# Kernel optimization log

Measured on AMD Instinct MI355X. Metric: run time of the kernel, lower is better.

## Reference

```python
import jax, jax.numpy as jnp
import numpy as np

H = 1024  # hidden_size
NH = 16   # num_attention_heads
HD = H // NH  # head_dim = 64


def setup_inputs() -> dict:
    key = jax.random.key(0)
    ks = jax.random.split(key, 9)
    s = 0.02
    return {
        "hidden_states": jax.random.normal(ks[0], (2, 2048, H), dtype=jnp.float32),
        "Wq": jax.random.normal(ks[1], (H, H), dtype=jnp.float32) * s,
        "bq": jnp.zeros((H,), dtype=jnp.float32),
        "Wk": jax.random.normal(ks[2], (H, H), dtype=jnp.float32) * s,
        "bk": jnp.zeros((H,), dtype=jnp.float32),
        "Wv": jax.random.normal(ks[3], (H, H), dtype=jnp.float32) * s,
        "bv": jnp.zeros((H,), dtype=jnp.float32),
        "Wo": jax.random.normal(ks[4], (H, H), dtype=jnp.float32) * s,
        "bo": jnp.zeros((H,), dtype=jnp.float32),
    }


def reference(hidden_states, Wq, bq, Wk, bk, Wv, bv, Wo, bo):
    B, S, _ = hidden_states.shape
    scale = 1.0 / np.sqrt(HD)
    # torch Linear: x @ W.T + b
    q = (hidden_states @ Wq.T + bq).reshape(B, S, NH, HD).transpose(0, 2, 1, 3)
    k = (hidden_states @ Wk.T + bk).reshape(B, S, NH, HD).transpose(0, 2, 1, 3)
    v = (hidden_states @ Wv.T + bv).reshape(B, S, NH, HD).transpose(0, 2, 1, 3)
    # full (non-causal) attention; tiled_matmul == plain matmul mathematically
    scores = jnp.einsum("bhqd,bhkd->bhqk", q, k) * scale
    attn = jax.nn.softmax(scores, axis=-1)
    out = jnp.einsum("bhqk,bhkd->bhqd", attn, v)
    out = out.transpose(0, 2, 1, 3).reshape(B, S, H)
    return out @ Wo.T + bo
```

## Files before the change

### kernel.cpp

```cpp
#include <hip/hip_runtime.h>

typedef unsigned short u16;
typedef __attribute__((ext_vector_type(8))) short bf16x8;
typedef __attribute__((ext_vector_type(4))) float f32x4;
typedef __attribute__((ext_vector_type(4))) unsigned int u32x4;

#define SEQ 2048
#define HID 1024
#define NHEAD 16
#define HDIM 64
#define MTOK 4096

#define MFMA16(a,b,c) __builtin_amdgcn_mfma_f32_16x16x32_bf16(a,b,c,0,0,0)

__device__ __forceinline__ u16 f2bf(float f){
  unsigned int u = __builtin_bit_cast(unsigned int, f);
  u += 0x7fffu + ((u >> 16) & 1u);
  return (u16)(u >> 16);
}

__device__ __forceinline__ void gload16(const u16* g, u16* l){
  __builtin_amdgcn_global_load_lds((const __attribute__((address_space(1))) void*)g,
                                   (__attribute__((address_space(3))) void*)l, 16, 0, 0);
}

__global__ __launch_bounds__(256) void cast_all(
    const float* __restrict__ hs, const float* __restrict__ Wq,
    const float* __restrict__ Wk, const float* __restrict__ Wv,
    const float* __restrict__ Wo, u16* __restrict__ Xb,
    u16* __restrict__ Wqkv, u16* __restrict__ Wob){
  int y = blockIdx.y;
  int i = blockIdx.x * 256 + threadIdx.x;
  const float* src; u16* dst; size_t i8;
  if (y < 4){ src = hs; dst = Xb; i8 = (size_t)y * 131072 + i; }
  else {
    int w = y - 4;
    src = (w == 0) ? Wq : (w == 1) ? Wk : (w == 2) ? Wv : Wo;
    dst = (w == 3) ? Wob : (Wqkv + (size_t)w * HID * HID);
    i8 = i;
  }
  const float4* p = (const float4*)src;
  float4 a = p[2*i8], b = p[2*i8+1];
  u32x4 o;
  o.x = (unsigned)f2bf(a.x) | ((unsigned)f2bf(a.y) << 16);
  o.y = (unsigned)f2bf(a.z) | ((unsigned)f2bf(a.w) << 16);
  o.z = (unsigned)f2bf(b.x) | ((unsigned)f2bf(b.y) << 16);
  o.w = (unsigned)f2bf(b.z) | ((unsigned)f2bf(b.w) << 16);
  ((u32x4*)dst)[i8] = o;
}

__global__ __launch_bounds__(256) void gemm_qkv(
    const u16* __restrict__ Xb, const u16* __restrict__ Wqkv,
    const float* __restrict__ bq, const float* __restrict__ bk, const float* __restrict__ bv,
    u16* __restrict__ Qb, u16* __restrict__ Kb, u16* __restrict__ Vtb)
{
  __shared__ __attribute__((aligned(16))) u16 pool[24576];
  u16* const AsP = pool;
  u16* const BsP = pool + 12288;
  const int tid = threadIdx.x, wave = tid >> 6, lane = tid & 63;
  const int m0 = blockIdx.x * 128, n0 = blockIdx.y * 128;
  const int wr = (wave >> 1) * 64, wc = (wave & 1) * 64;
  const int lr = lane & 15, lg = lane >> 4, kseg = lg * 8;

#define STAGE_Q(k0, buf) do { \
  _Pragma("unroll") \
  for (int i_ = 0; i_ < 2; i_++){ \
    int u_ = (i_*4 + wave) * 64 + lane; \
    int row_ = u_ >> 2, cu_ = u_ & 3; \
    gload16(Xb   + (size_t)(m0 + row_) * HID + (k0) + cu_*8, AsP + (buf)*4096 + (i_*4 + wave) * 512); \
    gload16(Wqkv + (size_t)(n0 + row_) * HID + (k0) + cu_*8, BsP + (buf)*4096 + (i_*4 + wave) * 512); \
  } } while(0)

  f32x4 zero = {0.f, 0.f, 0.f, 0.f};
  f32x4 acc[4][4];
#pragma unroll
  for (int i = 0; i < 4; i++)
#pragma unroll
    for (int j = 0; j < 4; j++) acc[i][j] = zero;

  STAGE_Q(0, 0);
  STAGE_Q(32, 1);
  for (int t = 0; t < 32; t++){
    if (t < 31) { asm volatile("s_waitcnt vmcnt(4)" ::: "memory"); }
    else        { asm volatile("s_waitcnt vmcnt(0)" ::: "memory"); }
    __builtin_amdgcn_s_barrier();
    __builtin_amdgcn_sched_barrier(0);
    if (t < 30) STAGE_Q((t+2)*32, (t+2)%3);
    int cur = t % 3;
    const u16* Ac = AsP + cur*4096; const u16* Bc = BsP + cur*4096;
    bf16x8 af[4], bfr[4];
#pragma unroll
    for (int m = 0; m < 4; m++) af[m]  = *(const bf16x8*)&Ac[(wr + m*16 + lr)*32 + kseg];
#pragma unroll
    for (int n = 0; n < 4; n++) bfr[n] = *(const bf16x8*)&Bc[(wc + n*16 + lr)*32 + kseg];
    __builtin_amdgcn_s_setprio(1);
#pragma unroll
    for (int m = 0; m < 4; m++)
#pragma unroll
      for (int n = 0; n < 4; n++)
        acc[m][n] = MFMA16(af[m], bfr[n], acc[m][n]);
    __builtin_amdgcn_s_setprio(0);
  }

  __syncthreads();
  const int sel = n0 >> 10;
  const float* bias = (sel == 0) ? bq : (sel == 1) ? bk : bv;
  const float qscale = (sel == 0) ? 0.18033688011f : 1.0f;
  u16* const Ct = pool;
#pragma unroll
  for (int n = 0; n < 4; n++){
    int colL = wc + n*16 + lr;
    float bb = bias[(n0 + colL) & 1023];
#pragma unroll
    for (int m = 0; m < 4; m++){
      int rowL = wr + m*16 + lg*4;
#pragma unroll
      for (int r = 0; r < 4; r++){
        u16 v = f2bf((acc[m][n][r] + bb) * qscale);
        if (sel == 2) Ct[(size_t)colL*136 + rowL + r] = v;
        else          Ct[(size_t)(rowL + r)*136 + colL] = v;
      }
    }
  }
  __syncthreads();
  const int hbase = (n0 & 1023) >> 6;
  if (sel < 2){
    int sl = tid & 127, hh = tid >> 7;
    int rowg = m0 + sl, b = rowg >> 11, s = rowg & 2047;
    u16* dst = ((sel == 0) ? Qb : Kb) + (((size_t)(b*16 + hbase + hh))*SEQ + s)*HDIM;
    const u16* srcl = Ct + (size_t)sl*136 + hh*64;
#pragma unroll
    for (int j = 0; j < 8; j++)
      *(u32x4*)(dst + j*8) = *(const u32x4*)(srcl + j*8);
  } else {
    int dcol = tid >> 1, sh = tid & 1;
    int b = m0 >> 11, s0 = (m0 & 2047) + sh*64;
    int h = hbase + (dcol >> 6), d = dcol & 63;
    u16* dst = Vtb + (((size_t)(b*16 + h))*HDIM + d)*SEQ + s0;
    const u16* srcl = Ct + (size_t)dcol*136 + sh*64;
#pragma unroll
    for (int j = 0; j < 8; j++)
      *(u32x4*)(dst + j*8) = *(const u32x4*)(srcl + j*8);
  }
}

__global__ __launch_bounds__(256) void attn_kernel(
    const u16* __restrict__ Qb, const u16* __restrict__ Kb, const u16* __restrict__ Vtb,
    u16* __restrict__ AOb)
{
  __shared__ __attribute__((aligned(16))) u16 Ks[3][64*64];
  __shared__ __attribute__((aligned(16))) u16 Vs[3][64*64];
  const int tid = threadIdx.x, wave = tid >> 6, lane = tid & 63;
  const int lr = lane & 15, lg = lane >> 4;
  const int bid = blockIdx.x;
  const int xcd = bid & 7, slot = bid >> 3;
  const int bh = xcd*4 + (slot >> 4);
  const int q0 = (slot & 15) * 128;
  const u16* Qh = Qb  + (size_t)bh * SEQ * HDIM;
  const u16* Kh = Kb  + (size_t)bh * SEQ * HDIM;
  const u16* Vh = Vtb + (size_t)bh * HDIM * SEQ;

#define STAGE_KV(kv0, buf) do { \
  _Pragma("unroll") \
  for (int i_ = 0; i_ < 2; i_++){ \
    int u_ = i_*256 + tid; \
    int r_ = u_ >> 3, s_ = u_ & 7, ss_ = s_ ^ (r_ & 7); \
    gload16(Kh + (size_t)((kv0) + r_) * HDIM + ss_*8, &Ks[buf][u_*8]); \
    gload16(Vh + (size_t)r_ * SEQ + (kv0) + ss_*8,    &Vs[buf][u_*8]); \
  } } while(0)

  bf16x8 qf[2][2];
#pragma unroll
  for (int qb = 0; qb < 2; qb++)
#pragma unroll
    for (int ks = 0; ks < 2; ks++)
      qf[qb][ks] = *(const bf16x8*)&Qh[(size_t)(q0 + wave*32 + qb*16 + lr) * HDIM + ks*32 + lg*8];

  f32x4 zero = {0.f, 0.f, 0.f, 0.f};
  f32x4 acc[2][4];
#pragma unroll
  for (int qb = 0; qb < 2; qb++)
#pragma unroll
    for (int fd = 0; fd < 4; fd++) acc[qb][fd] = zero;
  float m_c[2] = {-1e30f, -1e30f};
  float l_c[2] = {0.f, 0.f};

  STAGE_KV(0, 0);
  STAGE_KV(64, 1);
  for (int t = 0; t < 32; t++){
    if (t < 31) { asm volatile("s_waitcnt vmcnt(4)" ::: "memory"); }
    else        { asm volatile("s_waitcnt vmcnt(0)" ::: "memory"); }
    __builtin_amdgcn_s_barrier();
    __builtin_amdgcn_sched_barrier(0);
    if (t < 30) STAGE_KV((t+2)*64, (t+2)%3);
    int cur = t % 3;
    const u16* Kc = &Ks[cur][0];
    const u16* Vc = &Vs[cur][0];

    f32x4 st[2][4];
    __builtin_amdgcn_s_setprio(1);
#pragma unroll
    for (int f = 0; f < 4; f++){
      bf16x8 kf0 = *(const bf16x8*)&Kc[(f*16 + lr)*64 + ((lg     ^ (lr & 7)) * 8)];
      bf16x8 kf1 = *(const bf16x8*)&Kc[(f*16 + lr)*64 + (((4+lg) ^ (lr & 7)) * 8)];
      st[0][f] = MFMA16(kf0, qf[0][0], zero);
      st[0][f] = MFMA16(kf1, qf[0][1], st[0][f]);
      st[1][f] = MFMA16(kf0, qf[1][0], zero);
      st[1][f] = MFMA16(kf1, qf[1][1], st[1][f]);
    }
    __builtin_amdgcn_s_setprio(0);

    float pm[2];
#pragma unroll
    for (int qb = 0; qb < 2; qb++){
      float a0 = fmaxf(fmaxf(st[qb][0][0], st[qb][0][1]), fmaxf(st[qb][0][2], st[qb][0][3]));
      float a1 = fmaxf(fmaxf(st[qb][1][0], st[qb][1][1]), fmaxf(st[qb][1][2], st[qb][1][3]));
      float a2 = fmaxf(fmaxf(st[qb][2][0], st[qb][2][1]), fmaxf(st[qb][2][2], st[qb][2][3]));
      float a3 = fmaxf(fmaxf(st[qb][3][0], st[qb][3][1]), fmaxf(st[qb][3][2], st[qb][3][3]));
      pm[qb] = fmaxf(fmaxf(a0, a1), fmaxf(a2, a3));
    }
    int need = (pm[0] > m_c[0] + 11.5f) || (pm[1] > m_c[1] + 11.5f);
    if (__any(need)){
#pragma unroll
      for (int qb = 0; qb < 2; qb++){
        float mt = pm[qb];
        mt = fmaxf(mt, __shfl_xor(mt, 16));
        mt = fmaxf(mt, __shfl_xor(mt, 32));
        float mn = fmaxf(m_c[qb], mt);
        float al = __builtin_amdgcn_exp2f(m_c[qb] - mn);
        m_c[qb] = mn;
        l_c[qb] *= al;
        float r0 = __shfl(al, lg*4 + 0), r1 = __shfl(al, lg*4 + 1);
        float r2 = __shfl(al, lg*4 + 2), r3 = __shfl(al, lg*4 + 3);
#pragma unroll
        for (int fd = 0; fd < 4; fd++){
          acc[qb][fd][0] *= r0; acc[qb][fd][1] *= r1;
          acc[qb][fd][2] *= r2; acc[qb][fd][3] *= r3;
        }
      }
    }

    bf16x8 pa[2][2];
#pragma unroll
    for (int qb = 0; qb < 2; qb++){
      unsigned w[4][2];
      float ssum = 0.f;
#pragma unroll
      for (int f = 0; f < 4; f++){
        float p0 = __builtin_amdgcn_exp2f(st[qb][f][0] - m_c[qb]);
        float p1 = __builtin_amdgcn_exp2f(st[qb][f][1] - m_c[qb]);
        float p2 = __builtin_amdgcn_exp2f(st[qb][f][2] - m_c[qb]);
        float p3 = __builtin_amdgcn_exp2f(st[qb][f][3] - m_c[qb]);
        ssum += (p0 + p1) + (p2 + p3);
        asm("v_cvt_pk_bf16_f32 %0, %1, %2" : "=v"(w[f][0]) : "v"(p0), "v"(p1));
        asm("v_cvt_pk_bf16_f32 %0, %1, %2" : "=v"(w[f][1]) : "v"(p2), "v"(p3));
      }
      l_c[qb] += ssum;
#pragma unroll
      for (int ks = 0; ks < 2; ks++){
        u32x4 aw;
#pragma unroll
        for (int rr = 0; rr < 2; rr++){
          unsigned X = w[2*ks][rr], Y = w[2*ks+1][rr];
          asm("v_permlane32_swap_b32 %0, %1" : "+v"(X), "+v"(Y));
          asm("v_permlane16_swap_b32 %0, %1" : "+v"(X), "+v"(Y));
          aw[rr] = X; aw[2 + rr] = Y;
        }
        pa[qb][ks] = __builtin_bit_cast(bf16x8, aw);
      }
    }

    __builtin_amdgcn_s_setprio(1);
#pragma unroll
    for (int ks = 0; ks < 2; ks++)
#pragma unroll
      for (int fd = 0; fd < 4; fd++){
        bf16x8 vf = *(const bf16x8*)&Vc[(fd*16 + lr)*64 + (((ks*4 + lg) ^ (lr & 7)) * 8)];
        acc[0][fd] = MFMA16(pa[0][ks], vf, acc[0][fd]);
        acc[1][fd] = MFMA16(pa[1][ks], vf, acc[1][fd]);
      }
    __builtin_amdgcn_s_setprio(0);
  }

  const int b = bh >> 4, h = bh & 15;
#pragma unroll
  for (int qb = 0; qb < 2; qb++){
    float lt = l_c[qb];
    lt += __shfl_xor(lt, 16);
    lt += __shfl_xor(lt, 32);
    float li[4];
#pragma unroll
    for (int r = 0; r < 4; r++) li[r] = 1.0f / __shfl(lt, lg*4 + r);
#pragma unroll
    for (int fd = 0; fd < 4; fd++){
      int d = h*64 + fd*16 + lr;
#pragma unroll
      for (int r = 0; r < 4; r++){
        int s = q0 + wave*32 + qb*16 + lg*4 + r;
        AOb[((size_t)(b*SEQ + s))*HID + d] = f2bf(acc[qb][fd][r] * li[r]);
      }
    }
  }
}

__global__ __launch_bounds__(256) void gemm_out(
    const u16* __restrict__ Ab, const u16* __restrict__ Wob,
    const float* __restrict__ bo, float* __restrict__ Out)
{
  __shared__ __attribute__((aligned(16))) u16 As[3][64*32];
  __shared__ __attribute__((aligned(16))) u16 Bs[3][128*32];
  const int tid = threadIdx.x, wave = tid >> 6, lane = tid & 63;
  const int m0 = blockIdx.x * 64, n0 = blockIdx.y * 128;
  const int wr = (wave >> 1) * 32, wc = (wave & 1) * 64;
  const int lr = lane & 15, lg = lane >> 4, kseg = lg * 8;

#define STAGE_O(k0, buf) do { \
  { int u_ = wave*64 + lane; \
    int row_ = u_ >> 2, cu_ = u_ & 3; \
    gload16(Ab + (size_t)(m0 + row_) * HID + (k0) + cu_*8, &As[buf][wave * 512]); } \
  _Pragma("unroll") \
  for (int i_ = 0; i_ < 2; i_++){ \
    int u_ = (i_*4 + wave) * 64 + lane; \
    int row_ = u_ >> 2, cu_ = u_ & 3; \
    gload16(Wob + (size_t)(n0 + row_) * HID + (k0) + cu_*8, &Bs[buf][(i_*4 + wave) * 512]); \
  } } while(0)

  f32x4 zero = {0.f, 0.f, 0.f, 0.f};
  f32x4 acc[2][4];
#pragma unroll
  for (int i = 0; i < 2; i++)
#pragma unroll
    for (int j = 0; j < 4; j++) acc[i][j] = zero;

  STAGE_O(0, 0);
  STAGE_O(32, 1);
  for (int t = 0; t < 32; t++){
    if (t < 31) { asm volatile("s_waitcnt vmcnt(3)" ::: "memory"); }
    else        { asm volatile("s_waitcnt vmcnt(0)" ::: "memory"); }
    __builtin_amdgcn_s_barrier();
    __builtin_amdgcn_sched_barrier(0);
    if (t < 30) STAGE_O((t+2)*32, (t+2)%3);
    int cur = t % 3;
    const u16* Ac = As[cur]; const u16* Bc = Bs[cur];
    bf16x8 af[2], bfr[4];
#pragma unroll
    for (int m = 0; m < 2; m++) af[m]  = *(const bf16x8*)&Ac[(wr + m*16 + lr)*32 + kseg];
#pragma unroll
    for (int n = 0; n < 4; n++) bfr[n] = *(const bf16x8*)&Bc[(wc + n*16 + lr)*32 + kseg];
    __builtin_amdgcn_s_setprio(1);
#pragma unroll
    for (int m = 0; m < 2; m++)
#pragma unroll
      for (int n = 0; n < 4; n++)
        acc[m][n] = MFMA16(af[m], bfr[n], acc[m][n]);
    __builtin_amdgcn_s_setprio(0);
  }

#pragma unroll
  for (int n = 0; n < 4; n++){
    int col = n0 + wc + n*16 + lr;
    float bb = bo[col];
#pragma unroll
    for (int m = 0; m < 2; m++){
      int rbase = m0 + wr + m*16 + lg*4;
#pragma unroll
      for (int r = 0; r < 4; r++)
        Out[(size_t)(rbase + r) * HID + col] = acc[m][n][r] + bb;
    }
  }
}

extern "C" void kernel_launch(void* const* d_in, const int* in_sizes, int n_in,
                              void* d_out, int out_size, void* d_ws, size_t ws_size,
                              hipStream_t stream){
  const float* hs = (const float*)d_in[0];
  const float* Wq = (const float*)d_in[1];
  const float* bq = (const float*)d_in[2];
  const float* Wk = (const float*)d_in[3];
  const float* bk = (const float*)d_in[4];
  const float* Wv = (const float*)d_in[5];
  const float* bv = (const float*)d_in[6];
  const float* Wo = (const float*)d_in[7];
  const float* bo = (const float*)d_in[8];
  float* Out = (float*)d_out;

  u16* Xb   = (u16*)d_ws;
  u16* Wqkv = Xb   + (size_t)MTOK * HID;
  u16* Wob  = Wqkv + (size_t)3 * HID * HID;
  u16* Qb   = Wob  + (size_t)HID * HID;
  u16* Kb   = Qb   + (size_t)MTOK * HID;
  u16* Vtb  = Kb   + (size_t)MTOK * HID;
  u16* AOb  = Vtb  + (size_t)MTOK * HID;

  cast_all<<<dim3(512, 8), 256, 0, stream>>>(hs, Wq, Wk, Wv, Wo, Xb, Wqkv, Wob);
  gemm_qkv<<<dim3(MTOK/128, 3*HID/128), 256, 0, stream>>>(Xb, Wqkv, bq, bk, bv, Qb, Kb, Vtb);
  attn_kernel<<<512, 256, 0, stream>>>(Qb, Kb, Vtb, AOb);
  gemm_out<<<dim3(MTOK/64, HID/128), 256, 0, stream>>>(AOb, Wob, bo, Out);
}
```

Baseline: 204.7 us.

## Load K/V tiles directly from global into registers, drop LDS staging

```diff
diff --git a/kernel.cpp b/kernel.cpp
--- a/kernel.cpp
+++ b/kernel.cpp
@@ -148,33 +148,40 @@
     const u16* __restrict__ Qb, const u16* __restrict__ Kb, const u16* __restrict__ Vtb,
     u16* __restrict__ AOb)
 {
-  __shared__ __attribute__((aligned(16))) u16 Ks[3][64*64];
-  __shared__ __attribute__((aligned(16))) u16 Vs[3][64*64];
   const int tid = threadIdx.x, wave = tid >> 6, lane = tid & 63;
   const int lr = lane & 15, lg = lane >> 4;
   const int bid = blockIdx.x;
   const int xcd = bid & 7, slot = bid >> 3;
   const int bh = xcd*4 + (slot >> 4);
-  const int q0 = (slot & 15) * 128;
+  const int q0 = (slot & 15) * 128 + wave*32;
   const u16* Qh = Qb  + (size_t)bh * SEQ * HDIM;
   const u16* Kh = Kb  + (size_t)bh * SEQ * HDIM;
   const u16* Vh = Vtb + (size_t)bh * HDIM * SEQ;
-
-#define STAGE_KV(kv0, buf) do { \
+  const u16* kb = Kh + lr*HDIM + lg*8;
+  const u16* vb = Vh + (size_t)lr*SEQ + lg*8;
+
+#define LOADK(D, kv0_) do { \
   _Pragma("unroll") \
-  for (int i_ = 0; i_ < 2; i_++){ \
-    int u_ = i_*256 + tid; \
-    int r_ = u_ >> 3, s_ = u_ & 7, ss_ = s_ ^ (r_ & 7); \
-    gload16(Kh + (size_t)((kv0) + r_) * HDIM + ss_*8, &Ks[buf][u_*8]); \
-    gload16(Vh + (size_t)r_ * SEQ + (kv0) + ss_*8,    &Vs[buf][u_*8]); \
-  } } while(0)
+  for (int f_ = 0; f_ < 4; f_++) \
+    _Pragma("unroll") \
+    for (int h_ = 0; h_ < 2; h_++) \
+      D[f_*2 + h_] = *(const u32x4*)(kb + (size_t)(kv0_)*HDIM + f_*16*HDIM + h_*32); \
+  } while(0)
+
+#define LOADV(kv0_) do { \
+  _Pragma("unroll") \
+  for (int fd_ = 0; fd_ < 4; fd_++) \
+    _Pragma("unroll") \
+    for (int ks_ = 0; ks_ < 2; ks_++) \
+      vv[fd_*2 + ks_] = *(const u32x4*)(vb + (size_t)fd_*16*SEQ + (kv0_) + ks_*32); \
+  } while(0)
 
   bf16x8 qf[2][2];
 #pragma unroll
   for (int qb = 0; qb < 2; qb++)
 #pragma unroll
     for (int ks = 0; ks < 2; ks++)
-      qf[qb][ks] = *(const bf16x8*)&Qh[(size_t)(q0 + wave*32 + qb*16 + lr) * HDIM + ks*32 + lg*8];
+      qf[qb][ks] = *(const bf16x8*)&Qh[(size_t)(q0 + qb*16 + lr) * HDIM + ks*32 + lg*8];
 
   f32x4 zero = {0.f, 0.f, 0.f, 0.f};
   f32x4 acc[2][4];
@@ -185,101 +192,97 @@
   float m_c[2] = {-1e30f, -1e30f};
   float l_c[2] = {0.f, 0.f};
 
-  STAGE_KV(0, 0);
-  STAGE_KV(64, 1);
-  for (int t = 0; t < 32; t++){
-    if (t < 31) { asm volatile("s_waitcnt vmcnt(4)" ::: "memory"); }
-    else        { asm volatile("s_waitcnt vmcnt(0)" ::: "memory"); }
-    __builtin_amdgcn_s_barrier();
-    __builtin_amdgcn_sched_barrier(0);
-    if (t < 30) STAGE_KV((t+2)*64, (t+2)%3);
-    int cur = t % 3;
-    const u16* Kc = &Ks[cur][0];
-    const u16* Vc = &Vs[cur][0];
-
-    f32x4 st[2][4];
-    __builtin_amdgcn_s_setprio(1);
-#pragma unroll
-    for (int f = 0; f < 4; f++){
-      bf16x8 kf0 = *(const bf16x8*)&Kc[(f*16 + lr)*64 + ((lg     ^ (lr & 7)) * 8)];
-      bf16x8 kf1 = *(const bf16x8*)&Kc[(f*16 + lr)*64 + (((4+lg) ^ (lr & 7)) * 8)];
-      st[0][f] = MFMA16(kf0, qf[0][0], zero);
-      st[0][f] = MFMA16(kf1, qf[0][1], st[0][f]);
-      st[1][f] = MFMA16(kf0, qf[1][0], zero);
-      st[1][f] = MFMA16(kf1, qf[1][1], st[1][f]);
-    }
-    __builtin_amdgcn_s_setprio(0);
-
-    float pm[2];
-#pragma unroll
-    for (int qb = 0; qb < 2; qb++){
-      float a0 = fmaxf(fmaxf(st[qb][0][0], st[qb][0][1]), fmaxf(st[qb][0][2], st[qb][0][3]));
-      float a1 = fmaxf(fmaxf(st[qb][1][0], st[qb][1][1]), fmaxf(st[qb][1][2], st[qb][1][3]));
-      float a2 = fmaxf(fmaxf(st[qb][2][0], st[qb][2][1]), fmaxf(st[qb][2][2], st[qb][2][3]));
-      float a3 = fmaxf(fmaxf(st[qb][3][0], st[qb][3][1]), fmaxf(st[qb][3][2], st[qb][3][3]));
-      pm[qb] = fmaxf(fmaxf(a0, a1), fmaxf(a2, a3));
-    }
-    int need = (pm[0] > m_c[0] + 11.5f) || (pm[1] > m_c[1] + 11.5f);
-    if (__any(need)){
-#pragma unroll
-      for (int qb = 0; qb < 2; qb++){
-        float mt = pm[qb];
-        mt = fmaxf(mt, __shfl_xor(mt, 16));
-        mt = fmaxf(mt, __shfl_xor(mt, 32));
-        float mn = fmaxf(m_c[qb], mt);
-        float al = __builtin_amdgcn_exp2f(m_c[qb] - mn);
-        m_c[qb] = mn;
-        l_c[qb] *= al;
-        float r0 = __shfl(al, lg*4 + 0), r1 = __shfl(al, lg*4 + 1);
-        float r2 = __shfl(al, lg*4 + 2), r3 = __shfl(al, lg*4 + 3);
-#pragma unroll
-        for (int fd = 0; fd < 4; fd++){
-          acc[qb][fd][0] *= r0; acc[qb][fd][1] *= r1;
-          acc[qb][fd][2] *= r2; acc[qb][fd][3] *= r3;
-        }
-      }
-    }
-
-    bf16x8 pa[2][2];
-#pragma unroll
-    for (int qb = 0; qb < 2; qb++){
-      unsigned w[4][2];
-      float ssum = 0.f;
-#pragma unroll
-      for (int f = 0; f < 4; f++){
-        float p0 = __builtin_amdgcn_exp2f(st[qb][f][0] - m_c[qb]);
-        float p1 = __builtin_amdgcn_exp2f(st[qb][f][1] - m_c[qb]);
-        float p2 = __builtin_amdgcn_exp2f(st[qb][f][2] - m_c[qb]);
-        float p3 = __builtin_amdgcn_exp2f(st[qb][f][3] - m_c[qb]);
-        ssum += (p0 + p1) + (p2 + p3);
-        asm("v_cvt_pk_bf16_f32 %0, %1, %2" : "=v"(w[f][0]) : "v"(p0), "v"(p1));
-        asm("v_cvt_pk_bf16_f32 %0, %1, %2" : "=v"(w[f][1]) : "v"(p2), "v"(p3));
-      }
-      l_c[qb] += ssum;
-#pragma unroll
-      for (int ks = 0; ks < 2; ks++){
-        u32x4 aw;
-#pragma unroll
-        for (int rr = 0; rr < 2; rr++){
-          unsigned X = w[2*ks][rr], Y = w[2*ks+1][rr];
-          asm("v_permlane32_swap_b32 %0, %1" : "+v"(X), "+v"(Y));
-          asm("v_permlane16_swap_b32 %0, %1" : "+v"(X), "+v"(Y));
-          aw[rr] = X; aw[2 + rr] = Y;
-        }
-        pa[qb][ks] = __builtin_bit_cast(bf16x8, aw);
-      }
-    }
-
-    __builtin_amdgcn_s_setprio(1);
-#pragma unroll
-    for (int ks = 0; ks < 2; ks++)
-#pragma unroll
-      for (int fd = 0; fd < 4; fd++){
-        bf16x8 vf = *(const bf16x8*)&Vc[(fd*16 + lr)*64 + (((ks*4 + lg) ^ (lr & 7)) * 8)];
-        acc[0][fd] = MFMA16(pa[0][ks], vf, acc[0][fd]);
-        acc[1][fd] = MFMA16(pa[1][ks], vf, acc[1][fd]);
-      }
-    __builtin_amdgcn_s_setprio(0);
+  u32x4 kA[8], kB[8], vv[8];
+
+#define TILE_STEP(KARR, kv0_, ...) do { \
+    LOADV(kv0_); \
+    f32x4 st[2][4]; \
+    __builtin_amdgcn_s_setprio(1); \
+    _Pragma("unroll") \
+    for (int f = 0; f < 4; f++){ \
+      bf16x8 kf0 = __builtin_bit_cast(bf16x8, KARR[f*2+0]); \
+      bf16x8 kf1 = __builtin_bit_cast(bf16x8, KARR[f*2+1]); \
+      st[0][f] = MFMA16(kf0, qf[0][0], zero); \
+      st[0][f] = MFMA16(kf1, qf[0][1], st[0][f]); \
+      st[1][f] = MFMA16(kf0, qf[1][0], zero); \
+      st[1][f] = MFMA16(kf1, qf[1][1], st[1][f]); \
+    } \
+    __builtin_amdgcn_s_setprio(0); \
+    __VA_ARGS__; \
+    float pm[2]; \
+    _Pragma("unroll") \
+    for (int qb = 0; qb < 2; qb++){ \
+      float a0 = fmaxf(fmaxf(st[qb][0][0], st[qb][0][1]), fmaxf(st[qb][0][2], st[qb][0][3])); \
+      float a1 = fmaxf(fmaxf(st[qb][1][0], st[qb][1][1]), fmaxf(st[qb][1][2], st[qb][1][3])); \
+      float a2 = fmaxf(fmaxf(st[qb][2][0], st[qb][2][1]), fmaxf(st[qb][2][2], st[qb][2][3])); \
+      float a3 = fmaxf(fmaxf(st[qb][3][0], st[qb][3][1]), fmaxf(st[qb][3][2], st[qb][3][3])); \
+      pm[qb] = fmaxf(fmaxf(a0, a1), fmaxf(a2, a3)); \
+    } \
+    int need = (pm[0] > m_c[0] + 11.5f) || (pm[1] > m_c[1] + 11.5f); \
+    if (__any(need)){ \
+      _Pragma("unroll") \
+      for (int qb = 0; qb < 2; qb++){ \
+        float mt = pm[qb]; \
+        mt = fmaxf(mt, __shfl_xor(mt, 16)); \
+        mt = fmaxf(mt, __shfl_xor(mt, 32)); \
+        float mn = fmaxf(m_c[qb], mt); \
+        float al = __builtin_amdgcn_exp2f(m_c[qb] - mn); \
+        m_c[qb] = mn; \
+        l_c[qb] *= al; \
+        float r0 = __shfl(al, lg*4 + 0), r1 = __shfl(al, lg*4 + 1); \
+        float r2 = __shfl(al, lg*4 + 2), r3 = __shfl(al, lg*4 + 3); \
+        _Pragma("unroll") \
+        for (int fd = 0; fd < 4; fd++){ \
+          acc[qb][fd][0] *= r0; acc[qb][fd][1] *= r1; \
+          acc[qb][fd][2] *= r2; acc[qb][fd][3] *= r3; \
+        } \
+      } \
+    } \
+    bf16x8 pa[2][2]; \
+    _Pragma("unroll") \
+    for (int qb = 0; qb < 2; qb++){ \
+      unsigned w[4][2]; \
+      float ssum = 0.f; \
+      _Pragma("unroll") \
+      for (int f = 0; f < 4; f++){ \
+        float p0 = __builtin_amdgcn_exp2f(st[qb][f][0] - m_c[qb]); \
+        float p1 = __builtin_amdgcn_exp2f(st[qb][f][1] - m_c[qb]); \
+        float p2 = __builtin_amdgcn_exp2f(st[qb][f][2] - m_c[qb]); \
+        float p3 = __builtin_amdgcn_exp2f(st[qb][f][3] - m_c[qb]); \
+        ssum += (p0 + p1) + (p2 + p3); \
+        asm("v_cvt_pk_bf16_f32 %0, %1, %2" : "=v"(w[f][0]) : "v"(p0), "v"(p1)); \
+        asm("v_cvt_pk_bf16_f32 %0, %1, %2" : "=v"(w[f][1]) : "v"(p2), "v"(p3)); \
+      } \
+      l_c[qb] += ssum; \
+      _Pragma("unroll") \
+      for (int ks = 0; ks < 2; ks++){ \
+        u32x4 aw; \
+        _Pragma("unroll") \
+        for (int rr = 0; rr < 2; rr++){ \
+          unsigned X = w[2*ks][rr], Y = w[2*ks+1][rr]; \
+          asm("v_permlane32_swap_b32 %0, %1" : "+v"(X), "+v"(Y)); \
+          asm("v_permlane16_swap_b32 %0, %1" : "+v"(X), "+v"(Y)); \
+          aw[rr] = X; aw[2 + rr] = Y; \
+        } \
+        pa[qb][ks] = __builtin_bit_cast(bf16x8, aw); \
+      } \
+    } \
+    __builtin_amdgcn_s_setprio(1); \
+    _Pragma("unroll") \
+    for (int ks = 0; ks < 2; ks++) \
+      _Pragma("unroll") \
+      for (int fd = 0; fd < 4; fd++){ \
+        bf16x8 vf = __builtin_bit_cast(bf16x8, vv[fd*2 + ks]); \
+        acc[0][fd] = MFMA16(pa[0][ks], vf, acc[0][fd]); \
+        acc[1][fd] = MFMA16(pa[1][ks], vf, acc[1][fd]); \
+      } \
+    __builtin_amdgcn_s_setprio(0); \
+  } while(0)
+
+  LOADK(kA, 0);
+  for (int t = 0; t < 32; t += 2){
+    TILE_STEP(kA, t*64,       LOADK(kB, (t+1)*64));
+    TILE_STEP(kB, (t+1)*64,   if (t < 30) LOADK(kA, (t+2)*64));
   }
 
   const int b = bh >> 4, h = bh & 15;
@@ -296,7 +299,7 @@
       int d = h*64 + fd*16 + lr;
 #pragma unroll
       for (int r = 0; r < 4; r++){
-        int s = q0 + wave*32 + qb*16 + lg*4 + r;
+        int s = q0 + qb*16 + lg*4 + r;
         AOb[((size_t)(b*SEQ + s))*HID + d] = f2bf(acc[qb][fd][r] * li[r]);
       }
     }
```

Result: slower. 266.7 us (+30.3%).
